# Optimization experiments

Hardware: AMD Instinct MI355X
Metric: run time of the kernel (lower is better)

Reference implementation:

```python
import jax, jax.numpy as jnp
import numpy as np

ANCHORS_ALL = jnp.array([[10.,13.],[16.,30.],[33.,23.],[30.,61.],[62.,45.],
                         [59.,119.],[116.,90.],[156.,198.],[373.,326.]], dtype=jnp.float32)
INDICES = jnp.array([0, 1, 2], dtype=jnp.int32)   # anchor indices of level 0
ANCH_LVL = ANCHORS_ALL[0:3]                        # [nA, 2] anchors for this level
STRIDE = 8.0
N_CLS = 80
NA = 3


def _bce_logits(x, t):
    # elementwise binary_cross_entropy_with_logits (same formula as torch)
    return jnp.maximum(x, 0.0) - x * t + jnp.log1p(jnp.exp(-jnp.abs(x)))


def _iou_cxcywh(a, b):
    # a: [..., 4], b: [..., 4] (broadcastable), boxes as (cx, cy, w, h)
    ax1, ax2 = a[..., 0] - a[..., 2] * 0.5, a[..., 0] + a[..., 2] * 0.5
    ay1, ay2 = a[..., 1] - a[..., 3] * 0.5, a[..., 1] + a[..., 3] * 0.5
    bx1, bx2 = b[..., 0] - b[..., 2] * 0.5, b[..., 0] + b[..., 2] * 0.5
    by1, by2 = b[..., 1] - b[..., 3] * 0.5, b[..., 1] + b[..., 3] * 0.5
    iw = jnp.clip(jnp.minimum(ax2, bx2) - jnp.maximum(ax1, bx1), 0.0)
    ih = jnp.clip(jnp.minimum(ay2, by2) - jnp.maximum(ay1, by1), 0.0)
    inter = iw * ih
    union = (ax2 - ax1) * (ay2 - ay1) + (bx2 - bx1) * (by2 - by1) - inter
    return inter / (union + 1e-16)


def setup_inputs() -> dict:
    key = jax.random.key(0)
    ks = jax.random.split(key, 7)
    nB, nA, nH, nW, G = 8, 3, 160, 160, 32
    t_bbox = jax.random.normal(ks[0], (nB, nA, nH, nW, 4), jnp.float32)
    conf_logits = jax.random.normal(ks[1], (nB, nA, nH, nW, 1), jnp.float32)
    cls_logits = jax.random.normal(ks[2], (nB, nA, nH, nW, N_CLS), jnp.float32)
    cxy = jax.random.uniform(ks[3], (nB, G, 2), jnp.float32, 20.0, 1260.0)
    wh = jax.random.uniform(ks[4], (nB, G, 2), jnp.float32, 5.0, 60.0)
    gt_bboxes = jnp.concatenate([cxy, wh], axis=-1)           # cxcywh
    gt_cls = jax.random.randint(ks[5], (nB, G), 0, N_CLS, jnp.int32)
    gt_mask = jax.random.uniform(ks[6], (nB, G)) < 0.8        # padded-GT validity
    return dict(t_bbox=t_bbox, conf_logits=conf_logits, cls_logits=cls_logits,
                gt_bboxes=gt_bboxes, gt_cls=gt_cls, gt_mask=gt_mask)


def reference(t_bbox, conf_logits, cls_logits, gt_bboxes, gt_cls, gt_mask):
    nB, nA, nH, nW, _ = t_bbox.shape
    N = nA * nH * nW
    # ---- bbox decode (torch does this on a detached copy) ----
    sig = jax.nn.sigmoid(jax.lax.stop_gradient(t_bbox))
    yv, xv = jnp.meshgrid(jnp.arange(nH), jnp.arange(nW), indexing='ij')
    grid = jnp.stack([xv, yv], axis=-1).astype(jnp.float32).reshape(1, 1, nH, nW, 2)
    p_xy = (sig[..., 0:2] * 2.0 - 0.5 + grid) * STRIDE
    p_wh = (sig[..., 2:4] * 2.0) ** 2 * ANCH_LVL.reshape(1, nA, 1, 1, 2)
    p_bbox = jnp.concatenate([p_xy, p_wh], axis=-1).reshape(nB, N, 4)
    p_conf = jax.nn.sigmoid(jax.lax.stop_gradient(conf_logits))       # [nB,nA,nH,nW,1]
    p_cls = jax.nn.sigmoid(jax.lax.stop_gradient(cls_logits))
    cls_score = jnp.max(p_cls, axis=-1, keepdims=True)
    cls_idx = jnp.argmax(p_cls, axis=-1).reshape(nB, N)
    score = (p_conf * cls_score).reshape(nB, N)
    # ---- per-GT best-anchor matching (vectorized over [nB, G]) ----
    gw, gh = gt_bboxes[..., 2], gt_bboxes[..., 3]
    aw, ah = ANCHORS_ALL[:, 0], ANCHORS_ALL[:, 1]
    inter = jnp.minimum(gw[..., None], aw) * jnp.minimum(gh[..., None], ah)
    union = (gw * gh)[..., None] + aw * ah - inter
    anch_idx = jnp.argmax(inter / (union + 1e-16), axis=-1)           # [nB,G]
    matched = jnp.any(anch_idx[..., None] == INDICES, axis=-1)
    valid = gt_mask & matched
    ta = (anch_idx % NA).astype(jnp.int32)
    ti = jnp.clip((gt_bboxes[..., 0] / STRIDE).astype(jnp.int32), 0, nW - 1)
    tj = jnp.clip((gt_bboxes[..., 1] / STRIDE).astype(jnp.int32), 0, nH - 1)
    b_idx = jnp.arange(nB)[:, None]
    t_bb = t_bbox[b_idx, ta, tj, ti]       # [nB,G,4]
    t_cl = cls_logits[b_idx, ta, tj, ti]   # [nB,G,C]
    tgt_xy = ((gt_bboxes[..., 0:2] / STRIDE) % 1.0 + 0.5) / 2.0
    tgt_wh = jnp.sqrt(gt_bboxes[..., 2:4] / ANCH_LVL[ta]) / 2.0
    vm = valid.astype(t_bbox.dtype)
    loss_xy = jnp.sum(vm * jnp.sum(_bce_logits(t_bb[..., 0:2], tgt_xy), axis=-1))
    loss_wh = jnp.sum(vm * jnp.sum(_bce_logits(t_bb[..., 2:4], tgt_wh), axis=-1))
    onehot = jax.nn.one_hot(gt_cls, N_CLS, dtype=t_bbox.dtype)
    loss_cls = jnp.sum(vm * jnp.mean(_bce_logits(t_cl, onehot), axis=-1))
    # ---- objectness target: max IoU of every decoded box with the GTs ----
    ious = _iou_cxcywh(p_bbox[:, :, None, :], gt_bboxes[:, None, :, :])  # [nB,N,G]
    ious = jnp.where(gt_mask[:, None, :], ious, -1.0)
    has_gt = jnp.any(gt_mask, axis=-1)
    tconf = jnp.where(has_gt[:, None], jnp.max(ious, axis=-1), 0.0)
    tconf = tconf.reshape(nB, nA, nH, nW, 1)
    loss_conf = jnp.sum(_bce_logits(conf_logits, tconf))
    loss = (loss_xy + loss_wh + loss_conf + loss_cls) / nB
    return p_bbox, cls_idx, score, loss
```

## Files before the change

### kernel.cpp

```cpp
#include <hip/hip_runtime.h>

#define NB 8
#define NA 3
#define NH 160
#define NW 160
#define NCLS 80
#define NGT 32
#define NPB (NA * NH * NW)
#define TOTAL (NB * NPB)
#define OFF_CLSIDX (TOTAL * 4)
#define OFF_SCORE  (TOTAL * 5)
#define OFF_LOSS   (TOTAL * 6)

#define F4_PER_ROW 20
#define LDS_ROW_F4 21

__device__ float g_acc;

__device__ __forceinline__ float det_sigmoid(float x) { return 1.0f / (1.0f + expf(-x)); }
__device__ __forceinline__ float det_bce(float x, float t) {
    return fmaxf(x, 0.0f) - x * t + log1pf(expf(-fabsf(x)));
}
__device__ __forceinline__ float det_aw3(int a) { return a == 0 ? 10.0f : (a == 1 ? 16.0f : 33.0f); }
__device__ __forceinline__ float det_ah3(int a) { return a == 0 ? 13.0f : (a == 1 ? 30.0f : 23.0f); }

__device__ __forceinline__ bool det_mask_is_u8(const void* p) {
    const unsigned int* w = (const unsigned int*)p;
    unsigned int acc = 0;
#pragma unroll
    for (int k = 0; k < 64; k++) acc |= (w[k] & 0xFFFFFF00u);
    return acc != 0;
}
__device__ __forceinline__ bool det_mask_at(const void* p, bool u8mode, int idx) {
    return u8mode ? (((const unsigned char*)p)[idx] != 0)
                  : (((const int*)p)[idx] != 0);
}

__global__ void det_zero_k() { g_acc = 0.0f; }

__global__ void det_gt_k(const float* __restrict__ t_bbox,
                         const float* __restrict__ cls_logits,
                         const float* __restrict__ gt_bboxes,
                         const int* __restrict__ gt_cls,
                         const void* __restrict__ gt_mask) {
    __shared__ int s_u8;
    if (threadIdx.x == 0) s_u8 = det_mask_is_u8(gt_mask) ? 1 : 0;
    __syncthreads();
    bool u8mode = (s_u8 != 0);

    int t = threadIdx.x;
    int b = t >> 5;
    int g = t & 31;
    float4 gtb = ((const float4*)gt_bboxes)[b * NGT + g];
    float cx = gtb.x, cy = gtb.y, gw = gtb.z, gh = gtb.w;

    const float aw9[9] = {10.f,16.f,33.f,30.f,62.f,59.f,116.f,156.f,373.f};
    const float ah9[9] = {13.f,30.f,23.f,61.f,45.f,119.f,90.f,198.f,326.f};
    float garea = gw * gh;
    int aidx = 0;
    float best = -1.0f;
#pragma unroll
    for (int k = 0; k < 9; k++) {
        float inter = fminf(gw, aw9[k]) * fminf(gh, ah9[k]);
        float uni = garea + aw9[k] * ah9[k] - inter;
        float r = inter / (uni + 1e-16f);
        if (r > best) { best = r; aidx = k; }
    }
    bool valid = det_mask_at(gt_mask, u8mode, b * NGT + g) && (aidx < NA);
    int ta = aidx % NA;
    int ti = min(max((int)(cx * 0.125f), 0), NW - 1);
    int tj = min(max((int)(cy * 0.125f), 0), NH - 1);
    size_t cell = ((size_t)(b * NA + ta) * NH + tj) * NW + ti;

    float4 tb = ((const float4*)t_bbox)[cell];
    float fx = cx * 0.125f; fx -= floorf(fx);
    float fy = cy * 0.125f; fy -= floorf(fy);
    float tx = (fx + 0.5f) * 0.5f;
    float ty = (fy + 0.5f) * 0.5f;
    float tw = sqrtf(gw / det_aw3(ta)) * 0.5f;
    float th = sqrtf(gh / det_ah3(ta)) * 0.5f;

    float l = det_bce(tb.x, tx) + det_bce(tb.y, ty) +
              det_bce(tb.z, tw) + det_bce(tb.w, th);

    const float4* cl = (const float4*)(cls_logits + cell * NCLS);
    int tc = gt_cls[b * NGT + g];
    float lc = 0.0f;
#pragma unroll
    for (int c4 = 0; c4 < NCLS / 4; c4++) {
        float4 v = cl[c4];
        int c = c4 * 4;
        lc += det_bce(v.x, (c + 0 == tc) ? 1.0f : 0.0f);
        lc += det_bce(v.y, (c + 1 == tc) ? 1.0f : 0.0f);
        lc += det_bce(v.z, (c + 2 == tc) ? 1.0f : 0.0f);
        lc += det_bce(v.w, (c + 3 == tc) ? 1.0f : 0.0f);
    }
    l += lc * (1.0f / NCLS);
    if (valid) atomicAdd(&g_acc, l);
}

__global__ __launch_bounds__(256) void det_main_k(
    const float* __restrict__ t_bbox,
    const float* __restrict__ conf_logits,
    const float* __restrict__ cls_logits,
    const float* __restrict__ gt_bboxes,
    const void* __restrict__ gt_mask,
    float* __restrict__ out) {
    __shared__ float4 s_cls[4][16 * LDS_ROW_F4];
    __shared__ float s_x1[NGT], s_y1[NGT], s_x2[NGT], s_y2[NGT], s_ar[NGT];
    __shared__ float s_m[NGT];
    __shared__ float s_part[4];
    __shared__ int s_u8;

    int tid = threadIdx.x;
    int blockCell = blockIdx.x * 256;
    int gid = blockCell + tid;
    int b = gid / NPB;
    int r = gid % NPB;

    if (tid == 0) s_u8 = det_mask_is_u8(gt_mask) ? 1 : 0;
    __syncthreads();
    if (tid < NGT) {
        int g = tid;
        float4 gtb = ((const float4*)gt_bboxes)[b * NGT + g];
        s_x1[g] = gtb.x - gtb.z * 0.5f;
        s_x2[g] = gtb.x + gtb.z * 0.5f;
        s_y1[g] = gtb.y - gtb.w * 0.5f;
        s_y2[g] = gtb.y + gtb.w * 0.5f;
        s_ar[g] = gtb.z * gtb.w;
        s_m[g]  = det_mask_at(gt_mask, s_u8 != 0, b * NGT + g) ? 1.0f : 0.0f;
    }
    __syncthreads();

    int a   = r / (NH * NW);
    int rem = r % (NH * NW);
    int j   = rem / NW;
    int i   = rem % NW;

    float4 tb = ((const float4*)t_bbox)[gid];
    float s0 = det_sigmoid(tb.x), s1 = det_sigmoid(tb.y);
    float s2 = det_sigmoid(tb.z), s3 = det_sigmoid(tb.w);
    float px = (s0 * 2.0f - 0.5f + (float)i) * 8.0f;
    float py = (s1 * 2.0f - 0.5f + (float)j) * 8.0f;
    float sw = s2 * 2.0f, sh = s3 * 2.0f;
    float pw = sw * sw * det_aw3(a);
    float ph = sh * sh * det_ah3(a);
    float4 pb; pb.x = px; pb.y = py; pb.z = pw; pb.w = ph;
    ((float4*)out)[gid] = pb;

    float px1 = px - pw * 0.5f, px2 = px + pw * 0.5f;
    float py1 = py - ph * 0.5f, py2 = py + ph * 0.5f;
    float parea = pw * ph;
    float maxiou = 0.0f;
#pragma unroll
    for (int g = 0; g < NGT; g++) {
        float iw = fmaxf(fminf(px2, s_x2[g]) - fmaxf(px1, s_x1[g]), 0.0f);
        float ih = fmaxf(fminf(py2, s_y2[g]) - fmaxf(py1, s_y1[g]), 0.0f);
        float inter = iw * ih;
        float uni = parea + s_ar[g] - inter;
        float iou = inter / (uni + 1e-16f);
        maxiou = fmaxf(maxiou, (s_m[g] != 0.0f) ? iou : 0.0f);
    }

    float confl = conf_logits[gid];
    float sconf = det_sigmoid(confl);
    float lconf = det_bce(confl, maxiou);
#pragma unroll
    for (int off = 32; off > 0; off >>= 1) lconf += __shfl_down(lconf, off, 64);
    int w = tid >> 6, l = tid & 63;
    if (l == 0) s_part[w] = lconf;
    __syncthreads();
    if (tid == 0)
        atomicAdd(&g_acc, s_part[0] + s_part[1] + s_part[2] + s_part[3]);

    int cl_ = l >> 2;
    int q   = l & 3;
    const float4* g4 = (const float4*)cls_logits;
    int wbase = blockCell + w * 64;

#pragma unroll
    for (int it = 0; it < 4; ++it) {
        int tileCell = wbase + it * 16;
        size_t f4base = (size_t)tileCell * F4_PER_ROW;
        __syncthreads();
#pragma unroll
        for (int k = 0; k < 5; ++k) {
            int f = k * 64 + l;
            float4 v = g4[f4base + f];
            int rr = f / F4_PER_ROW;
            int cc = f - rr * F4_PER_ROW;
            s_cls[w][rr * LDS_ROW_F4 + cc] = v;
        }
        __syncthreads();

        float mx = -1e30f;
        int mi = 0;
#pragma unroll
        for (int k = 0; k < 5; ++k) {
            int col = q * 5 + k;
            float4 v = s_cls[w][cl_ * LDS_ROW_F4 + col];
            int c = col * 4;
            if (v.x > mx) { mx = v.x; mi = c + 0; }
            if (v.y > mx) { mx = v.y; mi = c + 1; }
            if (v.z > mx) { mx = v.z; mi = c + 2; }
            if (v.w > mx) { mx = v.w; mi = c + 3; }
        }
#pragma unroll
        for (int s = 1; s < 4; s <<= 1) {
            float ov = __shfl_xor(mx, s, 64);
            int   oi = __shfl_xor(mi, s, 64);
            if (ov > mx || (ov == mx && oi < mi)) { mx = ov; mi = oi; }
        }
        float sc = __shfl(sconf, it * 16 + cl_, 64);
        if (q == 0) {
            int cellg = tileCell + cl_;
            out[OFF_CLSIDX + cellg] = (float)mi;
            out[OFF_SCORE  + cellg] = sc * det_sigmoid(mx);
        }
    }
}

__global__ void det_fin_k(float* __restrict__ out) {
    out[OFF_LOSS] = g_acc * (1.0f / NB);
}

extern "C" void kernel_launch(void* const* d_in, const int* in_sizes, int n_in,
                              void* d_out, int out_size, void* d_ws, size_t ws_size,
                              hipStream_t stream) {
    (void)in_sizes; (void)n_in; (void)out_size; (void)d_ws; (void)ws_size;
    const float* t_bbox      = (const float*)d_in[0];
    const float* conf_logits = (const float*)d_in[1];
    const float* cls_logits  = (const float*)d_in[2];
    const float* gt_bboxes   = (const float*)d_in[3];
    const int*   gt_cls      = (const int*)d_in[4];
    const void*  gt_mask     = (const void*)d_in[5];
    float* out = (float*)d_out;

    det_zero_k<<<1, 1, 0, stream>>>();
    det_gt_k<<<1, 256, 0, stream>>>(t_bbox, cls_logits, gt_bboxes, gt_cls, gt_mask);
    det_main_k<<<TOTAL / 256, 256, 0, stream>>>(t_bbox, conf_logits, cls_logits,
                                                gt_bboxes, gt_mask, out);
    det_fin_k<<<1, 1, 0, stream>>>(out);
}
```

Measured before the change: 329.7 us.

## Fuse four launches into one kernel with last-block loss finalization

Merges the zero, GT-loss, main and finalize kernels into a single launch. Block 0 computes the GT matching loss, and a last-block-done counter writes the final loss and resets the accumulators for the next call. Block-wide barriers in the class-argmax loop are dropped because each wave uses its own LDS slice, and the GT box data is packed into float4/float2 shared arrays. The cost removed is the launch overhead and serialization of three tiny kernels. In exchange it adds a counter atomic per block and extra serial work in block 0.

Measured after the change: 412.6 us. 1.25x slower.

```diff
diff --git a/kernel.cpp b/kernel.cpp
--- a/kernel.cpp
+++ b/kernel.cpp
@@ -8,6 +8,7 @@
 #define NGT 32
 #define NPB (NA * NH * NW)
 #define TOTAL (NB * NPB)
+#define NBLK (TOTAL / 256)
 #define OFF_CLSIDX (TOTAL * 4)
 #define OFF_SCORE  (TOTAL * 5)
 #define OFF_LOSS   (TOTAL * 6)
@@ -15,7 +16,8 @@
 #define F4_PER_ROW 20
 #define LDS_ROW_F4 21
 
-__device__ float g_acc;
+__device__ float g_acc = 0.0f;
+__device__ unsigned int g_cnt = 0u;
 
 __device__ __forceinline__ float det_sigmoid(float x) { return 1.0f / (1.0f + expf(-x)); }
 __device__ __forceinline__ float det_bce(float x, float t) {
@@ -36,21 +38,15 @@
                   : (((const int*)p)[idx] != 0);
 }
 
-__global__ void det_zero_k() { g_acc = 0.0f; }
-
-__global__ void det_gt_k(const float* __restrict__ t_bbox,
-                         const float* __restrict__ cls_logits,
-                         const float* __restrict__ gt_bboxes,
-                         const int* __restrict__ gt_cls,
-                         const void* __restrict__ gt_mask) {
-    __shared__ int s_u8;
-    if (threadIdx.x == 0) s_u8 = det_mask_is_u8(gt_mask) ? 1 : 0;
-    __syncthreads();
-    bool u8mode = (s_u8 != 0);
-
-    int t = threadIdx.x;
-    int b = t >> 5;
-    int g = t & 31;
+__device__ __forceinline__ float det_gt_loss(int tid,
+        const float* __restrict__ t_bbox,
+        const float* __restrict__ cls_logits,
+        const float* __restrict__ gt_bboxes,
+        const int* __restrict__ gt_cls,
+        const void* __restrict__ gt_mask) {
+    bool u8mode = det_mask_is_u8(gt_mask);
+    int b = tid >> 5;
+    int g = tid & 31;
     float4 gtb = ((const float4*)gt_bboxes)[b * NGT + g];
     float cx = gtb.x, cy = gtb.y, gw = gtb.z, gh = gtb.w;
 
@@ -96,21 +92,21 @@
         lc += det_bce(v.w, (c + 3 == tc) ? 1.0f : 0.0f);
     }
     l += lc * (1.0f / NCLS);
-    if (valid) atomicAdd(&g_acc, l);
-}
-
-__global__ __launch_bounds__(256) void det_main_k(
+    return valid ? l : 0.0f;
+}
+
+__global__ __launch_bounds__(256) void det_all_k(
     const float* __restrict__ t_bbox,
     const float* __restrict__ conf_logits,
     const float* __restrict__ cls_logits,
     const float* __restrict__ gt_bboxes,
+    const int* __restrict__ gt_cls,
     const void* __restrict__ gt_mask,
     float* __restrict__ out) {
     __shared__ float4 s_cls[4][16 * LDS_ROW_F4];
-    __shared__ float s_x1[NGT], s_y1[NGT], s_x2[NGT], s_y2[NGT], s_ar[NGT];
-    __shared__ float s_m[NGT];
+    __shared__ float4 s_box[NGT];
+    __shared__ float2 s_am[NGT];
     __shared__ float s_part[4];
-    __shared__ int s_u8;
 
     int tid = threadIdx.x;
     int blockCell = blockIdx.x * 256;
@@ -118,17 +114,19 @@
     int b = gid / NPB;
     int r = gid % NPB;
 
-    if (tid == 0) s_u8 = det_mask_is_u8(gt_mask) ? 1 : 0;
-    __syncthreads();
     if (tid < NGT) {
-        int g = tid;
-        float4 gtb = ((const float4*)gt_bboxes)[b * NGT + g];
-        s_x1[g] = gtb.x - gtb.z * 0.5f;
-        s_x2[g] = gtb.x + gtb.z * 0.5f;
-        s_y1[g] = gtb.y - gtb.w * 0.5f;
-        s_y2[g] = gtb.y + gtb.w * 0.5f;
-        s_ar[g] = gtb.z * gtb.w;
-        s_m[g]  = det_mask_at(gt_mask, s_u8 != 0, b * NGT + g) ? 1.0f : 0.0f;
+        bool u8mode = det_mask_is_u8(gt_mask);
+        float4 gtb = ((const float4*)gt_bboxes)[b * NGT + tid];
+        float4 bx;
+        bx.x = gtb.x - gtb.z * 0.5f;
+        bx.y = gtb.y - gtb.w * 0.5f;
+        bx.z = gtb.x + gtb.z * 0.5f;
+        bx.w = gtb.y + gtb.w * 0.5f;
+        s_box[tid] = bx;
+        float2 am;
+        am.x = gtb.z * gtb.w;
+        am.y = det_mask_at(gt_mask, u8mode, b * NGT + tid) ? 1.0f : 0.0f;
+        s_am[tid] = am;
     }
     __syncthreads();
 
@@ -154,24 +152,27 @@
     float maxiou = 0.0f;
 #pragma unroll
     for (int g = 0; g < NGT; g++) {
-        float iw = fmaxf(fminf(px2, s_x2[g]) - fmaxf(px1, s_x1[g]), 0.0f);
-        float ih = fmaxf(fminf(py2, s_y2[g]) - fmaxf(py1, s_y1[g]), 0.0f);
+        float4 bx = s_box[g];
+        float2 am = s_am[g];
+        float iw = fmaxf(fminf(px2, bx.z) - fmaxf(px1, bx.x), 0.0f);
+        float ih = fmaxf(fminf(py2, bx.w) - fmaxf(py1, bx.y), 0.0f);
         float inter = iw * ih;
-        float uni = parea + s_ar[g] - inter;
+        float uni = parea + am.x - inter;
         float iou = inter / (uni + 1e-16f);
-        maxiou = fmaxf(maxiou, (s_m[g] != 0.0f) ? iou : 0.0f);
+        maxiou = fmaxf(maxiou, (am.y != 0.0f) ? iou : 0.0f);
     }
 
     float confl = conf_logits[gid];
     float sconf = det_sigmoid(confl);
     float lconf = det_bce(confl, maxiou);
+
+    if (blockIdx.x == 0)
+        lconf += det_gt_loss(tid, t_bbox, cls_logits, gt_bboxes, gt_cls, gt_mask);
+
 #pragma unroll
     for (int off = 32; off > 0; off >>= 1) lconf += __shfl_down(lconf, off, 64);
     int w = tid >> 6, l = tid & 63;
     if (l == 0) s_part[w] = lconf;
-    __syncthreads();
-    if (tid == 0)
-        atomicAdd(&g_acc, s_part[0] + s_part[1] + s_part[2] + s_part[3]);
 
     int cl_ = l >> 2;
     int q   = l & 3;
@@ -182,7 +183,6 @@
     for (int it = 0; it < 4; ++it) {
         int tileCell = wbase + it * 16;
         size_t f4base = (size_t)tileCell * F4_PER_ROW;
-        __syncthreads();
 #pragma unroll
         for (int k = 0; k < 5; ++k) {
             int f = k * 64 + l;
@@ -191,7 +191,6 @@
             int cc = f - rr * F4_PER_ROW;
             s_cls[w][rr * LDS_ROW_F4 + cc] = v;
         }
-        __syncthreads();
 
         float mx = -1e30f;
         int mi = 0;
@@ -218,10 +217,20 @@
             out[OFF_SCORE  + cellg] = sc * det_sigmoid(mx);
         }
     }
-}
-
-__global__ void det_fin_k(float* __restrict__ out) {
-    out[OFF_LOSS] = g_acc * (1.0f / NB);
+
+    __syncthreads();
+    if (tid == 0) {
+        atomicAdd(&g_acc, s_part[0] + s_part[1] + s_part[2] + s_part[3]);
+        __threadfence();
+        unsigned int t = atomicAdd(&g_cnt, 1u);
+        if (t == NBLK - 1) {
+            __threadfence();
+            float tot = atomicAdd(&g_acc, 0.0f);
+            out[OFF_LOSS] = tot * (1.0f / NB);
+            atomicExch(&g_acc, 0.0f);
+            atomicExch(&g_cnt, 0u);
+        }
+    }
 }
 
 extern "C" void kernel_launch(void* const* d_in, const int* in_sizes, int n_in,
@@ -236,9 +245,6 @@
     const void*  gt_mask     = (const void*)d_in[5];
     float* out = (float*)d_out;
 
-    det_zero_k<<<1, 1, 0, stream>>>();
-    det_gt_k<<<1, 256, 0, stream>>>(t_bbox, cls_logits, gt_bboxes, gt_cls, gt_mask);
-    det_main_k<<<TOTAL / 256, 256, 0, stream>>>(t_bbox, conf_logits, cls_logits,
-                                                gt_bboxes, gt_mask, out);
-    det_fin_k<<<1, 1, 0, stream>>>(out);
-}
+    det_all_k<<<NBLK, 256, 0, stream>>>(t_bbox, conf_logits, cls_logits,
+                                        gt_bboxes, gt_cls, gt_mask, out);
+}
```
